# Kernel optimization log

Measured on AMD Instinct MI355X. Metric: run time of the kernel, lower is better.

The kernel has to match this reference:

```python
import jax, jax.numpy as jnp
import numpy as np

N = 100000
E = 1600000
IN_FEAT = 128
OUT_FEAT = 64
ALPHA = 0.2  # LeakyReLU negative slope


def _xavier_uniform(key, shape, gain):
    fan_in, fan_out = shape[0], shape[1]
    limit = gain * np.sqrt(6.0 / (fan_in + fan_out))
    return jax.random.uniform(key, shape, jnp.float32, -limit, limit)


def setup_inputs() -> dict:
    key = jax.random.key(0)
    kx, ke, kw, ka = jax.random.split(key, 4)
    x = jax.random.normal(kx, (N, IN_FEAT), jnp.float32)
    edge = jax.random.randint(ke, (2, E), 0, N, jnp.int64 if jax.config.jax_enable_x64 else jnp.int32)
    W = _xavier_uniform(kw, (IN_FEAT, OUT_FEAT), 1.414)
    a = _xavier_uniform(ka, (1, 2 * OUT_FEAT), 1.414)
    return {"x": x, "W": W, "a": a, "edge": edge}


def reference(x, W, a, edge):
    n = x.shape[0]
    src, dst = edge[0], edge[1]
    h = x @ W                                  # [N, F]
    # a @ cat(h[src], h[dst]).T == (h @ a[:, :F].T)[src] + (h @ a[:, F:].T)[dst]
    a1 = a[0, :OUT_FEAT]
    a2 = a[0, OUT_FEAT:]
    score = (h @ a1)[src] + (h @ a2)[dst]       # [E]
    edge_e = jnp.exp(-jax.nn.leaky_relu(score, ALPHA))
    # sparse A (A[src,dst]=edge_e) @ ones -> row sums over outgoing edges of src
    e_rowsum = jax.ops.segment_sum(edge_e, src, num_segments=n)          # [N]
    # sparse A @ h -> out[i] = sum_{(i,j) in E} e_ij * h[j]
    h_prime = jax.ops.segment_sum(edge_e[:, None] * h[dst], src, num_segments=n)  # [N, F]
    h_prime = h_prime / e_rowsum[:, None]
    return jax.nn.elu(h_prime)  # concat=True
```

## Files before the change

kernel.cpp:

```cpp
#include <hip/hip_runtime.h>

#define IN_FEAT 128
#define OUT_FEAT 64
#define LRELU_ALPHA 0.2f
#define BUK_SHIFT 7
#define BUK_SIZE 128
#define MAX_NBUK 1024
#define D_BITS 17
#define D_MASK 0x1FFFF
#define BIN_THREADS 512
#define BIN_PER_THREAD 16
#define SLOT 2560
#define CAP 2560
#define STAGE_MAX 5
#define GEMM_ROWS 128

typedef __attribute__((ext_vector_type(8))) short bf16x8;
typedef __attribute__((ext_vector_type(4))) float floatx4;

__device__ __forceinline__ short f2bf(float f) {
  union { float f; unsigned u; } v; v.f = f;
  unsigned r = v.u + 0x7fff + ((v.u >> 16) & 1);
  return (short)(r >> 16);
}
__device__ __forceinline__ float bf2f(unsigned short s) {
  union { unsigned u; float f; } v; v.u = ((unsigned)s) << 16;
  return v.f;
}

union SMemU {
  struct { __align__(16) short Wt[64 * 136]; float a_sh[2 * OUT_FEAT]; } g;
  struct { int lhist[MAX_NBUK]; int lbase[MAX_NBUK]; } b;
};

__global__ __launch_bounds__(512) void gemm_bin_kernel(
    const float* __restrict__ x, const float* __restrict__ W,
    const float* __restrict__ a, unsigned short* __restrict__ h,
    float* __restrict__ s1, float* __restrict__ s2, int N,
    const int* __restrict__ src, const int* __restrict__ dst,
    int* __restrict__ cursor, int* __restrict__ bukdata, int E,
    int grid_bin) {
  __shared__ SMemU sm;

  int t = threadIdx.x;

  if (blockIdx.x < grid_bin) {
    for (int i = t; i < MAX_NBUK; i += BIN_THREADS) sm.b.lhist[i] = 0;
    __syncthreads();
    int base_e = blockIdx.x * (BIN_THREADS * BIN_PER_THREAD);
#pragma unroll
    for (int j = 0; j < BIN_PER_THREAD; ++j) {
      int e = base_e + j * BIN_THREADS + t;
      if (e < E) atomicAdd(&sm.b.lhist[src[e] >> BUK_SHIFT], 1);
    }
    __syncthreads();
    for (int i = t; i < MAX_NBUK; i += BIN_THREADS) {
      int c = sm.b.lhist[i];
      sm.b.lbase[i] = c > 0 ? atomicAdd(&cursor[i], c) : 0;
      sm.b.lhist[i] = 0;
    }
    __syncthreads();
#pragma unroll
    for (int j = 0; j < BIN_PER_THREAD; ++j) {
      int e = base_e + j * BIN_THREADS + t;
      if (e < E) {
        int sv = src[e];
        int b = sv >> BUK_SHIFT;
        int pos = sm.b.lbase[b] + atomicAdd(&sm.b.lhist[b], 1);
        if (pos < SLOT)
          bukdata[b * SLOT + pos] = ((sv & (BUK_SIZE - 1)) << D_BITS) | dst[e];
      }
    }
    return;
  }

  if (t < 2 * OUT_FEAT) sm.g.a_sh[t] = a[t];
  for (int i = t; i < IN_FEAT * OUT_FEAT; i += 512) {
    int k = i >> 6, n = i & 63;
    sm.g.Wt[n * 136 + k] = f2bf(W[i]);
  }
  __syncthreads();

  int wave = t >> 6;
  int lane = t & 63;
  int l = lane & 15;
  int quad = lane >> 4;

  int row_base = (blockIdx.x - grid_bin) * GEMM_ROWS + wave * 16;
  int m = row_base + l;
  int m_c = m < N ? m : N - 1;

  bf16x8 bfrag[4][4];
#pragma unroll
  for (int kt = 0; kt < 4; ++kt)
#pragma unroll
    for (int nt = 0; nt < 4; ++nt)
      bfrag[kt][nt] = *(const bf16x8*)&sm.g.Wt[(nt * 16 + l) * 136 + kt * 32 + quad * 8];

  floatx4 acc[4] = {floatx4{0,0,0,0}, floatx4{0,0,0,0}, floatx4{0,0,0,0}, floatx4{0,0,0,0}};
  const float* xrow = x + (size_t)m_c * IN_FEAT;
#pragma unroll
  for (int kt = 0; kt < 4; ++kt) {
    float4 xa = *(const float4*)(xrow + kt * 32 + quad * 8);
    float4 xb = *(const float4*)(xrow + kt * 32 + quad * 8 + 4);
    bf16x8 af;
    af[0] = f2bf(xa.x); af[1] = f2bf(xa.y); af[2] = f2bf(xa.z); af[3] = f2bf(xa.w);
    af[4] = f2bf(xb.x); af[5] = f2bf(xb.y); af[6] = f2bf(xb.z); af[7] = f2bf(xb.w);
#pragma unroll
    for (int nt = 0; nt < 4; ++nt)
      acc[nt] = __builtin_amdgcn_mfma_f32_16x16x32_bf16(af, bfrag[kt][nt], acc[nt], 0, 0, 0);
  }

  int out_row = row_base + quad * 4;
#pragma unroll
  for (int reg = 0; reg < 4; ++reg) {
    int r = out_row + reg;
    if (r < N) {
#pragma unroll
      for (int nt = 0; nt < 4; ++nt)
        h[(size_t)r * OUT_FEAT + nt * 16 + l] = (unsigned short)f2bf(acc[nt][reg]);
    }
  }

  float p1[4] = {0, 0, 0, 0}, p2[4] = {0, 0, 0, 0};
#pragma unroll
  for (int nt = 0; nt < 4; ++nt) {
    float a1v = sm.g.a_sh[nt * 16 + l];
    float a2v = sm.g.a_sh[OUT_FEAT + nt * 16 + l];
#pragma unroll
    for (int reg = 0; reg < 4; ++reg) {
      p1[reg] += acc[nt][reg] * a1v;
      p2[reg] += acc[nt][reg] * a2v;
    }
  }
#pragma unroll
  for (int off = 1; off < 16; off <<= 1) {
#pragma unroll
    for (int reg = 0; reg < 4; ++reg) {
      p1[reg] += __shfl_xor(p1[reg], off);
      p2[reg] += __shfl_xor(p2[reg], off);
    }
  }
  if (l < 4) {
    int r = out_row + l;
    if (r < N) {
      float v1 = l == 0 ? p1[0] : (l == 1 ? p1[1] : (l == 2 ? p1[2] : p1[3]));
      float v2 = l == 0 ? p2[0] : (l == 1 ? p2[1] : (l == 2 ? p2[2] : p2[3]));
      s1[r] = v1;
      s2[r] = v2;
    }
  }
}

__global__ __launch_bounds__(512) void bucket_sort_aggregate_kernel(
    const int* __restrict__ bukdata, const int* __restrict__ cursor,
    const float* __restrict__ s1, const float* __restrict__ s2,
    const unsigned short* __restrict__ h, float* __restrict__ out, int N) {
  __shared__ float s1sh[BUK_SIZE];
  __shared__ int lhist[BUK_SIZE];
  __shared__ int loffs[BUK_SIZE];
  __shared__ int lcur[BUK_SIZE];
  __shared__ int wtot[2];
  __shared__ int2 lrec[CAP];

  int t = threadIdx.x;
  int buk = blockIdx.x;
  int beg = buk * SLOT;
  int cnt_total = min(cursor[buk], SLOT);
  int end = beg + cnt_total;
  int node_base = buk << BUK_SHIFT;

  if (t < BUK_SIZE) {
    int ng = node_base + t;
    s1sh[t] = ng < N ? s1[ng] : 0.f;
  }

  int wid = t >> 6;
  int lane = t & 63;
  int half = lane >> 5;
  int c2 = lane & 31;

  float ax[16], ay[16], rs[16];
#pragma unroll
  for (int j = 0; j < 16; ++j) { ax[j] = 0.f; ay[j] = 0.f; rs[j] = 0.f; }

  for (int cbeg = beg; cbeg < end; cbeg += CAP) {
    int cnt = min(end - cbeg, CAP);

    if (t < BUK_SIZE) lhist[t] = 0;
    __syncthreads();

    int dreg[STAGE_MAX];
    int slreg[STAGE_MAX];
    float ereg[STAGE_MAX];
#pragma unroll
    for (int j = 0; j < STAGE_MAX; ++j) {
      int i = t + j * 512;
      bool v = i < cnt;
      int pk = v ? bukdata[cbeg + i] : 0;
      slreg[j] = pk >> D_BITS;
      dreg[j] = pk & D_MASK;
      float sc = s1sh[slreg[j]] + (v ? s2[dreg[j]] : 0.f);
      ereg[j] = __expf(-(sc > 0.f ? sc : LRELU_ALPHA * sc));
      if (v) atomicAdd(&lhist[slreg[j]], 1);
    }
    __syncthreads();

    int hv = (t < BUK_SIZE) ? lhist[t] : 0;
    int xs = hv;
#pragma unroll
    for (int off = 1; off < 64; off <<= 1) {
      int y = __shfl_up(xs, off);
      if (lane >= off) xs += y;
    }
    if (t < BUK_SIZE && lane == 63) wtot[t >> 6] = xs;
    __syncthreads();
    if (t < BUK_SIZE) {
      int base = (t >> 6) ? wtot[0] : 0;
      int excl = base + xs - hv;
      loffs[t] = excl;
      lcur[t] = excl;
    }
    __syncthreads();

#pragma unroll
    for (int j = 0; j < STAGE_MAX; ++j) {
      int i = t + j * 512;
      if (i < cnt) {
        int pos = atomicAdd(&lcur[slreg[j]], 1);
        lrec[pos] = make_int2(dreg[j], __float_as_int(ereg[j]));
      }
    }
    __syncthreads();

#pragma unroll
    for (int p = 0; p < 8; ++p) {
      int nlA = wid + (2 * p) * 8;
      int nlB = wid + (2 * p + 1) * 8;
      int cA = lhist[nlA];
      int cB = lhist[nlB];
      int oA = cA > 0 ? loffs[nlA] : 0;
      int oB = cB > 0 ? loffs[nlB] : 0;
      int kmax = cA > cB ? cA : cB;
      for (int k = 0; k < kmax; k += 8) {
#pragma unroll
        for (int j = 0; j < 4; ++j) {
          int idx = k + 2 * j + half;
          bool vA = idx < cA;
          bool vB = idx < cB;
          int2 rA = lrec[oA + (vA ? idx : 0)];
          int2 rB = lrec[oB + (vB ? idx : 0)];
          float eA = vA ? __int_as_float(rA.y) : 0.f;
          float eB = vB ? __int_as_float(rB.y) : 0.f;
          unsigned hA = *(const unsigned*)&h[rA.x * OUT_FEAT + 2 * c2];
          unsigned hB = *(const unsigned*)&h[rB.x * OUT_FEAT + 2 * c2];
          rs[2 * p]     += eA;
          ax[2 * p]     += eA * bf2f(hA & 0xffff);
          ay[2 * p]     += eA * bf2f(hA >> 16);
          rs[2 * p + 1] += eB;
          ax[2 * p + 1] += eB * bf2f(hB & 0xffff);
          ay[2 * p + 1] += eB * bf2f(hB >> 16);
        }
      }
    }
    __syncthreads();
  }

#pragma unroll
  for (int nn = 0; nn < 16; ++nn) {
    float r = rs[nn] + __shfl_xor(rs[nn], 32);
    float xv = ax[nn] + __shfl_xor(ax[nn], 32);
    float yv = ay[nn] + __shfl_xor(ay[nn], 32);
    int ng = node_base + wid + nn * 8;
    if (ng < N && half == 0) {
      float vx = xv / r, vy = yv / r;
      vx = vx > 0.f ? vx : __expf(vx) - 1.f;
      vy = vy > 0.f ? vy : __expf(vy) - 1.f;
      *(float2*)&out[(size_t)ng * OUT_FEAT + 2 * c2] = make_float2(vx, vy);
    }
  }
}

extern "C" void kernel_launch(void* const* d_in, const int* in_sizes, int n_in,
                              void* d_out, int out_size, void* d_ws, size_t ws_size,
                              hipStream_t stream) {
  const float* x = (const float*)d_in[0];
  const float* W = (const float*)d_in[1];
  const float* a = (const float*)d_in[2];
  const int* edge = (const int*)d_in[3];

  const int N = in_sizes[0] / IN_FEAT;
  const int E = in_sizes[3] / 2;
  const int* src = edge;
  const int* dst = edge + E;

  float* out = (float*)d_out;

  const int NB = (N + BUK_SIZE - 1) / BUK_SIZE;

  char* p = (char*)d_ws;
  unsigned short* h = (unsigned short*)p; p += (size_t)N * OUT_FEAT * sizeof(unsigned short);
  float* s1 = (float*)p;      p += (size_t)N * sizeof(float);
  float* s2 = (float*)p;      p += (size_t)N * sizeof(float);
  int* cursor = (int*)p;      p += MAX_NBUK * sizeof(int);
  int* bukdata = (int*)p;     p += (size_t)NB * SLOT * sizeof(int);

  hipMemsetAsync(cursor, 0, MAX_NBUK * sizeof(int), stream);

  int grid_bin = (E + BIN_THREADS * BIN_PER_THREAD - 1) / (BIN_THREADS * BIN_PER_THREAD);
  int grid_gemm = (N + GEMM_ROWS - 1) / GEMM_ROWS;
  gemm_bin_kernel<<<grid_bin + grid_gemm, 512, 0, stream>>>(
      x, W, a, h, s1, s2, N, src, dst, cursor, bukdata, E, grid_bin);

  bucket_sort_aggregate_kernel<<<NB, 512, 0, stream>>>(
      bukdata, cursor, s1, s2, h, out, N);
}
```

Baseline: 184.5 us.

## Remap aggregation to quarter-wave per node and drop chunk loop

Removes the multi-chunk outer loop, since SLOT equals CAP and each bucket holds at most one chunk. The aggregation is remapped so each 16-lane quarter of a wave handles one node and reads 4 bf16 features per lane (8-byte loads). Each wave now covers 4 nodes at once instead of two halves splitting edges, which removes the cross-half shuffle reduction and cuts register accumulators from 48 to 5. In exchange, the loop bound is the max edge count over 4 nodes, which adds divergence padding, and h gathers become narrower per node.

```diff
diff --git a/kernel.cpp b/kernel.cpp
--- a/kernel.cpp
+++ b/kernel.cpp
@@ -166,117 +166,95 @@
   int t = threadIdx.x;
   int buk = blockIdx.x;
   int beg = buk * SLOT;
-  int cnt_total = min(cursor[buk], SLOT);
-  int end = beg + cnt_total;
+  int cnt = min(cursor[buk], SLOT);
   int node_base = buk << BUK_SHIFT;
 
   if (t < BUK_SIZE) {
     int ng = node_base + t;
     s1sh[t] = ng < N ? s1[ng] : 0.f;
-  }
+    lhist[t] = 0;
+  }
+  __syncthreads();
 
   int wid = t >> 6;
   int lane = t & 63;
-  int half = lane >> 5;
-  int c2 = lane & 31;
-
-  float ax[16], ay[16], rs[16];
-#pragma unroll
-  for (int j = 0; j < 16; ++j) { ax[j] = 0.f; ay[j] = 0.f; rs[j] = 0.f; }
-
-  for (int cbeg = beg; cbeg < end; cbeg += CAP) {
-    int cnt = min(end - cbeg, CAP);
-
-    if (t < BUK_SIZE) lhist[t] = 0;
-    __syncthreads();
-
-    int dreg[STAGE_MAX];
-    int slreg[STAGE_MAX];
-    float ereg[STAGE_MAX];
-#pragma unroll
-    for (int j = 0; j < STAGE_MAX; ++j) {
-      int i = t + j * 512;
-      bool v = i < cnt;
-      int pk = v ? bukdata[cbeg + i] : 0;
-      slreg[j] = pk >> D_BITS;
-      dreg[j] = pk & D_MASK;
-      float sc = s1sh[slreg[j]] + (v ? s2[dreg[j]] : 0.f);
-      ereg[j] = __expf(-(sc > 0.f ? sc : LRELU_ALPHA * sc));
-      if (v) atomicAdd(&lhist[slreg[j]], 1);
-    }
-    __syncthreads();
-
-    int hv = (t < BUK_SIZE) ? lhist[t] : 0;
-    int xs = hv;
-#pragma unroll
-    for (int off = 1; off < 64; off <<= 1) {
-      int y = __shfl_up(xs, off);
-      if (lane >= off) xs += y;
-    }
-    if (t < BUK_SIZE && lane == 63) wtot[t >> 6] = xs;
-    __syncthreads();
-    if (t < BUK_SIZE) {
-      int base = (t >> 6) ? wtot[0] : 0;
-      int excl = base + xs - hv;
-      loffs[t] = excl;
-      lcur[t] = excl;
-    }
-    __syncthreads();
-
-#pragma unroll
-    for (int j = 0; j < STAGE_MAX; ++j) {
-      int i = t + j * 512;
-      if (i < cnt) {
-        int pos = atomicAdd(&lcur[slreg[j]], 1);
-        lrec[pos] = make_int2(dreg[j], __float_as_int(ereg[j]));
+
+  int dreg[STAGE_MAX];
+  int slreg[STAGE_MAX];
+  float ereg[STAGE_MAX];
+#pragma unroll
+  for (int j = 0; j < STAGE_MAX; ++j) {
+    int i = t + j * 512;
+    bool v = i < cnt;
+    int pk = v ? bukdata[beg + i] : 0;
+    slreg[j] = pk >> D_BITS;
+    dreg[j] = pk & D_MASK;
+    float sc = s1sh[slreg[j]] + (v ? s2[dreg[j]] : 0.f);
+    ereg[j] = __expf(-(sc > 0.f ? sc : LRELU_ALPHA * sc));
+    if (v) atomicAdd(&lhist[slreg[j]], 1);
+  }
+  __syncthreads();
+
+  int hv = (t < BUK_SIZE) ? lhist[t] : 0;
+  int xs = hv;
+#pragma unroll
+  for (int off = 1; off < 64; off <<= 1) {
+    int y = __shfl_up(xs, off);
+    if (lane >= off) xs += y;
+  }
+  if (t < BUK_SIZE && lane == 63) wtot[t >> 6] = xs;
+  __syncthreads();
+  if (t < BUK_SIZE) {
+    int base = (t >> 6) ? wtot[0] : 0;
+    int excl = base + xs - hv;
+    loffs[t] = excl;
+    lcur[t] = excl;
+  }
+  __syncthreads();
+
+#pragma unroll
+  for (int j = 0; j < STAGE_MAX; ++j) {
+    int i = t + j * 512;
+    if (i < cnt) {
+      int pos = atomicAdd(&lcur[slreg[j]], 1);
+      lrec[pos] = make_int2(dreg[j], __float_as_int(ereg[j]));
+    }
+  }
+  __syncthreads();
+
+  int quad = lane >> 4;
+  int ql = lane & 15;
+#pragma unroll
+  for (int jj = 0; jj < 4; ++jj) {
+    int nl = wid + 32 * quad + 8 * jj;
+    int c = lhist[nl];
+    int o = c > 0 ? loffs[nl] : 0;
+    int cm = max(c, __shfl_xor(c, 16));
+    cm = max(cm, __shfl_xor(cm, 32));
+    float a0 = 0.f, a1 = 0.f, a2 = 0.f, a3 = 0.f, rsum = 0.f;
+    for (int k = 0; k < cm; k += 8) {
+#pragma unroll
+      for (int u = 0; u < 8; ++u) {
+        int idx = k + u;
+        bool v = idx < c;
+        int2 r = lrec[o + (v ? idx : 0)];
+        float ee = v ? __int_as_float(r.y) : 0.f;
+        uint2 hvv = *(const uint2*)&h[r.x * OUT_FEAT + ql * 4];
+        a0 += ee * bf2f((unsigned short)(hvv.x & 0xffff));
+        a1 += ee * bf2f((unsigned short)(hvv.x >> 16));
+        a2 += ee * bf2f((unsigned short)(hvv.y & 0xffff));
+        a3 += ee * bf2f((unsigned short)(hvv.y >> 16));
+        rsum += ee;
       }
     }
-    __syncthreads();
-
-#pragma unroll
-    for (int p = 0; p < 8; ++p) {
-      int nlA = wid + (2 * p) * 8;
-      int nlB = wid + (2 * p + 1) * 8;
-      int cA = lhist[nlA];
-      int cB = lhist[nlB];
-      int oA = cA > 0 ? loffs[nlA] : 0;
-      int oB = cB > 0 ? loffs[nlB] : 0;
-      int kmax = cA > cB ? cA : cB;
-      for (int k = 0; k < kmax; k += 8) {
-#pragma unroll
-        for (int j = 0; j < 4; ++j) {
-          int idx = k + 2 * j + half;
-          bool vA = idx < cA;
-          bool vB = idx < cB;
-          int2 rA = lrec[oA + (vA ? idx : 0)];
-          int2 rB = lrec[oB + (vB ? idx : 0)];
-          float eA = vA ? __int_as_float(rA.y) : 0.f;
-          float eB = vB ? __int_as_float(rB.y) : 0.f;
-          unsigned hA = *(const unsigned*)&h[rA.x * OUT_FEAT + 2 * c2];
-          unsigned hB = *(const unsigned*)&h[rB.x * OUT_FEAT + 2 * c2];
-          rs[2 * p]     += eA;
-          ax[2 * p]     += eA * bf2f(hA & 0xffff);
-          ay[2 * p]     += eA * bf2f(hA >> 16);
-          rs[2 * p + 1] += eB;
-          ax[2 * p + 1] += eB * bf2f(hB & 0xffff);
-          ay[2 * p + 1] += eB * bf2f(hB >> 16);
-        }
-      }
-    }
-    __syncthreads();
-  }
-
-#pragma unroll
-  for (int nn = 0; nn < 16; ++nn) {
-    float r = rs[nn] + __shfl_xor(rs[nn], 32);
-    float xv = ax[nn] + __shfl_xor(ax[nn], 32);
-    float yv = ay[nn] + __shfl_xor(ay[nn], 32);
-    int ng = node_base + wid + nn * 8;
-    if (ng < N && half == 0) {
-      float vx = xv / r, vy = yv / r;
-      vx = vx > 0.f ? vx : __expf(vx) - 1.f;
-      vy = vy > 0.f ? vy : __expf(vy) - 1.f;
-      *(float2*)&out[(size_t)ng * OUT_FEAT + 2 * c2] = make_float2(vx, vy);
+    int ng = node_base + nl;
+    if (ng < N) {
+      float v0 = a0 / rsum, v1 = a1 / rsum, v2 = a2 / rsum, v3 = a3 / rsum;
+      v0 = v0 > 0.f ? v0 : __expf(v0) - 1.f;
+      v1 = v1 > 0.f ? v1 : __expf(v1) - 1.f;
+      v2 = v2 > 0.f ? v2 : __expf(v2) - 1.f;
+      v3 = v3 > 0.f ? v3 : __expf(v3) - 1.f;
+      *(float4*)&out[(size_t)ng * OUT_FEAT + ql * 4] = make_float4(v0, v1, v2, v3);
     }
   }
 }
```

Result: faster. 170.2 us (-7.8%).
